# Kernel tuning notes

Hardware: AMD Instinct MI355X
Metric: run time of the kernel (lower is better)

## Reference

```python
import jax, jax.numpy as jnp
import numpy as np

# Config constants (mirrors VQConfig)
N_CODEBOOKS = 4
NUM_EMBS = 512
EMB_DIM = 32
NUM_LATENTS = 64
DECAY = 0.999
COMMITMENT_COST = 0.25
EPSILON = 1e-05
BATCH = 1024


def setup_inputs() -> dict:
    key = jax.random.key(0)
    k1, k2 = jax.random.split(key)
    x = jax.random.normal(k1, (BATCH, N_CODEBOOKS * EMB_DIM * NUM_LATENTS), dtype=jnp.float32)
    # embedding.uniform_(-1/M*5, 1/M*5)
    lim = 5.0 / NUM_EMBS
    embedding = jax.random.uniform(k2, (N_CODEBOOKS, NUM_EMBS, EMB_DIM), dtype=jnp.float32,
                                   minval=-lim, maxval=lim)
    ema_count = jnp.zeros((N_CODEBOOKS, NUM_EMBS), dtype=jnp.float32)
    ema_weight = embedding  # clone of embedding at init
    return {"x": x, "embedding": embedding, "ema_count": ema_count, "ema_weight": ema_weight}


def reference(x, embedding, ema_count, ema_weight):
    N, M, D = embedding.shape
    B = x.shape[0]
    L = x.shape[1] // (N * D)  # num_discrete_latents (H dim; W = 1)
    T = B * L  # flattened positions per codebook

    # x.view(B, N*D, L, 1).view(B, N, D, H, W).permute(1,0,3,4,2) -> [N,B,L,1,D]
    xr = x.reshape(B, N, D, L, 1).transpose(1, 0, 3, 4, 2)
    x_flat = jax.lax.stop_gradient(xr).reshape(N, T, D)

    e_sq = jnp.sum(embedding ** 2, axis=2)                       # [N, M]
    x_sq = jnp.sum(x_flat ** 2, axis=2, keepdims=True)           # [N, T, 1]
    xe = jnp.einsum('ntd,nmd->ntm', x_flat, embedding)           # [N, T, M]
    distances = e_sq[:, None, :] + x_sq - 2.0 * xe
    indices = jnp.argmin(distances, axis=-1)                     # [N, T] int

    # gather: quantized[n, t] = embedding[n, indices[n, t]]
    quantized = jnp.take_along_axis(embedding, indices[..., None], axis=1)  # [N,T,D]
    quantized_r = quantized.reshape(N, B, L, 1, D)

    # one-hot sums without materializing one-hot: scatter-add via segment_sum
    flat_idx = (indices + jnp.arange(N, dtype=indices.dtype)[:, None] * M).reshape(-1)
    counts = jax.ops.segment_sum(jnp.ones((N * T,), jnp.float32), flat_idx,
                                 num_segments=N * M).reshape(N, M)
    dw = jax.ops.segment_sum(x_flat.reshape(N * T, D), flat_idx,
                             num_segments=N * M).reshape(N, M, D)

    # EMA updates (training branch)
    new_ema_count = DECAY * ema_count + (1.0 - DECAY) * counts
    n_tot = jnp.sum(new_ema_count, axis=-1, keepdims=True)
    new_ema_count = (new_ema_count + EPSILON) / (n_tot + M * EPSILON) * n_tot
    new_ema_weight = DECAY * ema_weight + (1.0 - DECAY) * dw
    new_embedding = new_ema_weight / new_ema_count[..., None]

    # commitment loss + straight-through estimator
    e_latent_loss = jnp.mean((xr - jax.lax.stop_gradient(quantized_r)) ** 2)
    loss = COMMITMENT_COST * e_latent_loss
    quantized_st = jax.lax.stop_gradient(quantized_r) + xr - jax.lax.stop_gradient(xr)

    # perplexity
    avg_probs = counts / T                                       # [N, M]
    perplexity = jnp.exp(-jnp.sum(avg_probs * jnp.log(avg_probs + 1e-10), axis=-1))
    perplexity_sum = jnp.sum(perplexity)

    # [N,B,L,1,D] -> permute(1,0,4,2,3) -> [B,N,D,L,1] -> flatten
    z_q = quantized_st.transpose(1, 0, 4, 2, 3).reshape(B, N * D * L)
    indices_out = indices.reshape(N, B, L, 1).transpose(1, 0, 2, 3)  # [B,N,L,1]

    return (z_q, loss, perplexity_sum, indices_out,
            new_embedding, new_ema_count, new_ema_weight)
```

## Files before the change

kernel.cpp:

```cpp
#include <hip/hip_runtime.h>

#define NCB 4
#define M 512
#define D 32
#define L 64
#define B 1024
#define XS (NCB * D * L)

#define ZQ_OFF   0
#define LOSS_OFF 8388608
#define PERP_OFF 8388609
#define IDX_OFF  8388610
#define NEMB_OFF 8650754
#define NEC_OFF  8716290
#define NWE_OFF  8718338

#define WS_COUNTS 0
#define WS_DW     2048
#define WS_SSE    67584
#define WS_ESQ    67585
#define WS_FLOATS (WS_ESQ + NCB * M)

#define REFINE_EPS 1e-4f

#define NP_SUM32(sq, res) do {                                              \
    float r0=(sq)[0], r1=(sq)[1], r2=(sq)[2], r3=(sq)[3];                   \
    float r4=(sq)[4], r5=(sq)[5], r6=(sq)[6], r7=(sq)[7];                   \
    r0 += (sq)[8];  r1 += (sq)[9];  r2 += (sq)[10]; r3 += (sq)[11];         \
    r4 += (sq)[12]; r5 += (sq)[13]; r6 += (sq)[14]; r7 += (sq)[15];         \
    r0 += (sq)[16]; r1 += (sq)[17]; r2 += (sq)[18]; r3 += (sq)[19];         \
    r4 += (sq)[20]; r5 += (sq)[21]; r6 += (sq)[22]; r7 += (sq)[23];         \
    r0 += (sq)[24]; r1 += (sq)[25]; r2 += (sq)[26]; r3 += (sq)[27];         \
    r4 += (sq)[28]; r5 += (sq)[29]; r6 += (sq)[30]; r7 += (sq)[31];         \
    (res) = ((r0 + r1) + (r2 + r3)) + ((r4 + r5) + (r6 + r7));              \
} while (0)

__global__ __launch_bounds__(256) void vq_esq(
    const float* __restrict__ emb, float* __restrict__ ws)
{
#pragma clang fp contract(off)
    const int r = blockIdx.x * 256 + threadIdx.x;
    const float* ep = emb + (size_t)r * D;
    float sq[D];
#pragma unroll
    for (int d = 0; d < D; ++d) { const float e = ep[d]; sq[d] = e * e; }
    float res;
    NP_SUM32(sq, res);
    ws[WS_ESQ + r] = res;
}

__global__ __launch_bounds__(256, 4) void vq_main(
    const float* __restrict__ x, const float* __restrict__ emb,
    const float* __restrict__ esq,
    float* __restrict__ out, float* __restrict__ ws)
{
#pragma clang fp contract(off)
    const int tid = threadIdx.x;
    const int lane = tid & 63;
    const int bid = blockIdx.x;
    const int n  = bid >> 8;
    const int t  = ((bid & 255) << 8) + tid;
    const float* __restrict__ embn = emb + n * (M * D);
    const float* __restrict__ esqn = esq + n * M;

    const int b = t >> 6, l = t & 63;
    float xr[D];
    {
        const float* xp = x + (size_t)b * XS + n * (D * L) + l;
#pragma unroll
        for (int d = 0; d < D; ++d) xr[d] = xp[d * L];
    }

    float xsq;
    {
        float sq[D];
#pragma unroll
        for (int d = 0; d < D; ++d) sq[d] = xr[d] * xr[d];
        NP_SUM32(sq, xsq);
    }

    float best = 3.4e38f, secnd = 3.4e38f;
    int   bi = 0;

    for (int m = 0; m < M; ++m) {
        const float* __restrict__ ep = embn + m * D;
        float a0 = 0.f, a1 = 0.f, a2 = 0.f, a3 = 0.f;
#pragma unroll
        for (int h = 0; h < D; h += 16) {
            a0 = fmaf(ep[h+ 0], xr[h+ 0], a0); a0 = fmaf(ep[h+ 1], xr[h+ 1], a0);
            a0 = fmaf(ep[h+ 2], xr[h+ 2], a0); a0 = fmaf(ep[h+ 3], xr[h+ 3], a0);
            a1 = fmaf(ep[h+ 4], xr[h+ 4], a1); a1 = fmaf(ep[h+ 5], xr[h+ 5], a1);
            a1 = fmaf(ep[h+ 6], xr[h+ 6], a1); a1 = fmaf(ep[h+ 7], xr[h+ 7], a1);
            a2 = fmaf(ep[h+ 8], xr[h+ 8], a2); a2 = fmaf(ep[h+ 9], xr[h+ 9], a2);
            a2 = fmaf(ep[h+10], xr[h+10], a2); a2 = fmaf(ep[h+11], xr[h+11], a2);
            a3 = fmaf(ep[h+12], xr[h+12], a3); a3 = fmaf(ep[h+13], xr[h+13], a3);
            a3 = fmaf(ep[h+14], xr[h+14], a3); a3 = fmaf(ep[h+15], xr[h+15], a3);
        }
        const float s = fmaf(-2.f, ((a0 + a1) + (a2 + a3)), esqn[m]);
        const bool lt = s < best;
        secnd = lt ? best : fminf(secnd, s);
        best  = lt ? s : best;
        bi    = lt ? m : bi;
    }

    {
        unsigned long long mask = __ballot(secnd - best < REFINE_EPS);
        while (mask) {
            const int src = __ffsll(mask) - 1;
            mask &= mask - 1;
            float xb[D];
#pragma unroll
            for (int d = 0; d < D; ++d) xb[d] = __shfl(xr[d], src, 64);
            const float xsb = __shfl(xsq, src, 64);
            float bs = 3.4e38f; int bm = M;
            for (int mb = 0; mb < 8; ++mb) {
                const int m = mb * 64 + lane;
                const float4* e4 = (const float4*)(embn + m * D);
                float ee[D];
#pragma unroll
                for (int q = 0; q < 8; ++q) {
                    const float4 v = e4[q];
                    ee[q*4+0] = v.x; ee[q*4+1] = v.y; ee[q*4+2] = v.z; ee[q*4+3] = v.w;
                }
                float lnk[4];
#pragma unroll
                for (int il = 0; il < 4; ++il) {
                    float c;
                    c = xb[12+il] * ee[12+il];
                    c = xb[ 8+il] * ee[ 8+il] + c;
                    c = xb[ 4+il] * ee[ 4+il] + c;
                    c = xb[ 0+il] * ee[ 0+il] + c;
                    c = xb[28+il] * ee[28+il] + c;
                    c = xb[24+il] * ee[24+il] + c;
                    c = xb[20+il] * ee[20+il] + c;
                    c = xb[16+il] * ee[16+il] + c;
                    lnk[il] = c;
                }
                const float xe   = (lnk[0] + lnk[1]) + (lnk[2] + lnk[3]);
                const float a1v  = esqn[m] + xsb;
                const float dist = a1v - 2.f * xe;
                if (dist < bs || (dist == bs && m < bm)) { bs = dist; bm = m; }
            }
#pragma unroll
            for (int off = 32; off > 0; off >>= 1) {
                const float os = __shfl_xor(bs, off, 64);
                const int   om = __shfl_xor(bm, off, 64);
                if (os < bs || (os == bs && om < bm)) { bs = os; bm = om; }
            }
            if (lane == src) bi = bm;
        }
    }

    float sse = 0.f;
    {
        const float* q = embn + bi * D;
        float* zq = out + ZQ_OFF + (size_t)b * XS + n * (D * L) + l;
#pragma unroll
        for (int d = 0; d < D; ++d) {
            const float qv = q[d];
            zq[d * L] = qv;
            const float diff = xr[d] - qv;
            sse = fmaf(diff, diff, sse);
        }
        out[IDX_OFF + ((size_t)b * NCB + n) * L + l] = (float)bi;
        unsafeAtomicAdd(&ws[WS_COUNTS + n * M + bi], 1.0f);
        float* dwp = ws + WS_DW + (size_t)(n * M + bi) * D;
#pragma unroll
        for (int d = 0; d < D; ++d) unsafeAtomicAdd(&dwp[d], xr[d]);
    }

#pragma unroll
    for (int off = 32; off > 0; off >>= 1) sse += __shfl_down(sse, off, 64);
    if (lane == 0) unsafeAtomicAdd(&ws[WS_SSE], sse);
}

__global__ __launch_bounds__(256) void vq_finalize(
    const float* __restrict__ ema_count, const float* __restrict__ ema_weight,
    const float* __restrict__ ws, float* __restrict__ out)
{
    const int n = blockIdx.x, tid = threadIdx.x;
    __shared__ float s_nec[M];
    __shared__ float s_red[16];

    float pre[2], tot = 0.f, ent = 0.f;
#pragma unroll
    for (int k = 0; k < 2; ++k) {
        const int m = tid + k * 256;
        const float c = ws[WS_COUNTS + n * M + m];
        pre[k] = 0.999f * ema_count[n * M + m] + 0.001f * c;
        tot += pre[k];
        const float p = c * (1.f / 65536.f);
        ent += p * logf(p + 1e-10f);
    }
#pragma unroll
    for (int off = 32; off > 0; off >>= 1) {
        tot += __shfl_down(tot, off, 64);
        ent += __shfl_down(ent, off, 64);
    }
    const int w = tid >> 6;
    if ((tid & 63) == 0) { s_red[w] = tot; s_red[8 + w] = ent; }
    __syncthreads();
    tot = s_red[0] + s_red[1] + s_red[2] + s_red[3];
    ent = s_red[8] + s_red[9] + s_red[10] + s_red[11];

    if (tid == 0) unsafeAtomicAdd(&out[PERP_OFF], expf(-ent));
    if (n == 0 && tid == 0) out[LOSS_OFF] = 0.25f * ws[WS_SSE] * (1.f / 8388608.f);

#pragma unroll
    for (int k = 0; k < 2; ++k) {
        const int m = tid + k * 256;
        const float nec = (pre[k] + 1e-5f) / (tot + M * 1e-5f) * tot;
        out[NEC_OFF + n * M + m] = nec;
        s_nec[m] = nec;
    }
    __syncthreads();

    for (int e = tid; e < M * D; e += 256) {
        const int m = e >> 5;
        const float wv = 0.999f * ema_weight[n * (M * D) + e] + 0.001f * ws[WS_DW + n * (M * D) + e];
        out[NWE_OFF + n * (M * D) + e] = wv;
        out[NEMB_OFF + n * (M * D) + e] = wv / s_nec[m];
    }
}

extern "C" void kernel_launch(void* const* d_in, const int* in_sizes, int n_in,
                              void* d_out, int out_size, void* d_ws, size_t ws_size,
                              hipStream_t stream) {
    const float* x          = (const float*)d_in[0];
    const float* embedding  = (const float*)d_in[1];
    const float* ema_count  = (const float*)d_in[2];
    const float* ema_weight = (const float*)d_in[3];
    float* out = (float*)d_out;
    float* ws  = (float*)d_ws;

    hipMemsetAsync(ws, 0, (WS_SSE + 1) * sizeof(float), stream);
    hipMemsetAsync((char*)d_out + (size_t)LOSS_OFF * sizeof(float), 0, 2 * sizeof(float), stream);

    vq_esq<<<dim3(NCB * M / 256), dim3(256), 0, stream>>>(embedding, ws);
    vq_main<<<dim3(1024), dim3(256), 0, stream>>>(x, embedding, ws + WS_ESQ, out, ws);
    vq_finalize<<<dim3(NCB), dim3(256), 0, stream>>>(ema_count, ema_weight, ws, out);
}
```

Measured before the change: 900.9 us.

## Replace global atomics for counts and dw with LDS-privatized stats kernel

Removes the per-position global atomic adds for code counts and dw sums from the main kernel. A new stats kernel re-reads the indices and x, accumulates dw in shared memory with swizzled atomics across 32 blocks (8 segments per codebook), and writes partial sums that finalize reduces. Counts are now rebuilt in finalize with shared-memory integer atomics. This cuts global atomic contention at the cost of an extra pass over x, an extra launch, and low parallelism (32 blocks for stats, 4 for finalize).

```diff
diff --git a/kernel.cpp b/kernel.cpp
--- a/kernel.cpp
+++ b/kernel.cpp
@@ -15,11 +15,11 @@
 #define NEC_OFF  8716290
 #define NWE_OFF  8718338
 
-#define WS_COUNTS 0
-#define WS_DW     2048
-#define WS_SSE    67584
-#define WS_ESQ    67585
-#define WS_FLOATS (WS_ESQ + NCB * M)
+#define WS_SSE   0
+#define WS_ESQ   1
+#define WS_DWP   (1 + NCB * M)
+#define SBLK     8
+#define SPOS     (65536 / SBLK)
 
 #define REFINE_EPS 1e-4f
 
@@ -163,15 +163,45 @@
             sse = fmaf(diff, diff, sse);
         }
         out[IDX_OFF + ((size_t)b * NCB + n) * L + l] = (float)bi;
-        unsafeAtomicAdd(&ws[WS_COUNTS + n * M + bi], 1.0f);
-        float* dwp = ws + WS_DW + (size_t)(n * M + bi) * D;
-#pragma unroll
-        for (int d = 0; d < D; ++d) unsafeAtomicAdd(&dwp[d], xr[d]);
-    }
-
+    }
 #pragma unroll
     for (int off = 32; off > 0; off >>= 1) sse += __shfl_down(sse, off, 64);
     if (lane == 0) unsafeAtomicAdd(&ws[WS_SSE], sse);
+}
+
+__global__ __launch_bounds__(256) void vq_stats(
+    const float* __restrict__ x, const float* __restrict__ out,
+    float* __restrict__ ws)
+{
+    __shared__ float dwl[M * D];
+    const int tid = threadIdx.x;
+    const int blk = blockIdx.x;
+    const int n = blk >> 3, seg = blk & 7;
+
+#pragma unroll
+    for (int k = 0; k < (M * D) / 256; ++k) dwl[tid + k * 256] = 0.f;
+    __syncthreads();
+
+    const int t0 = seg * SPOS;
+    for (int k = 0; k < SPOS / 256; ++k) {
+        const int t = t0 + k * 256 + tid;
+        const int b = t >> 6, l = t & 63;
+        const int m = (int)out[IDX_OFF + ((size_t)b * NCB + n) * L + l];
+        const float* xp = x + (size_t)b * XS + n * (D * L) + l;
+        const int base = m * D, sw = m & 31;
+#pragma unroll
+        for (int d = 0; d < D; ++d)
+            atomicAdd(&dwl[base + (d ^ sw)], xp[d * L]);
+    }
+    __syncthreads();
+
+    float* dst = ws + WS_DWP + (size_t)(n * SBLK + seg) * (M * D);
+#pragma unroll
+    for (int k = 0; k < (M * D) / 256; ++k) {
+        const int e = tid + k * 256;
+        const int m = e >> 5, d = e & 31;
+        dst[e] = dwl[(e & ~31) + (d ^ (m & 31))];
+    }
 }
 
 __global__ __launch_bounds__(256) void vq_finalize(
@@ -179,14 +209,27 @@
     const float* __restrict__ ws, float* __restrict__ out)
 {
     const int n = blockIdx.x, tid = threadIdx.x;
+    __shared__ int   s_cnt[M];
     __shared__ float s_nec[M];
     __shared__ float s_red[16];
 
+#pragma unroll
+    for (int k = 0; k < 2; ++k) s_cnt[tid + k * 256] = 0;
+    __syncthreads();
+
+    for (int k = 0; k < 65536 / 256; ++k) {
+        const int t = k * 256 + tid;
+        const int b = t >> 6, l = t & 63;
+        const int m = (int)out[IDX_OFF + ((size_t)b * NCB + n) * L + l];
+        atomicAdd(&s_cnt[m], 1);
+    }
+    __syncthreads();
+
     float pre[2], tot = 0.f, ent = 0.f;
 #pragma unroll
     for (int k = 0; k < 2; ++k) {
         const int m = tid + k * 256;
-        const float c = ws[WS_COUNTS + n * M + m];
+        const float c = (float)s_cnt[m];
         pre[k] = 0.999f * ema_count[n * M + m] + 0.001f * c;
         tot += pre[k];
         const float p = c * (1.f / 65536.f);
@@ -216,8 +259,12 @@
     __syncthreads();
 
     for (int e = tid; e < M * D; e += 256) {
+        float dwsum = 0.f;
+#pragma unroll
+        for (int p = 0; p < SBLK; ++p)
+            dwsum += ws[WS_DWP + (size_t)(n * SBLK + p) * (M * D) + e];
         const int m = e >> 5;
-        const float wv = 0.999f * ema_weight[n * (M * D) + e] + 0.001f * ws[WS_DW + n * (M * D) + e];
+        const float wv = 0.999f * ema_weight[n * (M * D) + e] + 0.001f * dwsum;
         out[NWE_OFF + n * (M * D) + e] = wv;
         out[NEMB_OFF + n * (M * D) + e] = wv / s_nec[m];
     }
@@ -233,10 +280,11 @@
     float* out = (float*)d_out;
     float* ws  = (float*)d_ws;
 
-    hipMemsetAsync(ws, 0, (WS_SSE + 1) * sizeof(float), stream);
+    hipMemsetAsync(ws + WS_SSE, 0, sizeof(float), stream);
     hipMemsetAsync((char*)d_out + (size_t)LOSS_OFF * sizeof(float), 0, 2 * sizeof(float), stream);
 
     vq_esq<<<dim3(NCB * M / 256), dim3(256), 0, stream>>>(embedding, ws);
     vq_main<<<dim3(1024), dim3(256), 0, stream>>>(x, embedding, ws + WS_ESQ, out, ws);
+    vq_stats<<<dim3(NCB * SBLK), dim3(256), 0, stream>>>(x, out, ws);
     vq_finalize<<<dim3(NCB), dim3(256), 0, stream>>>(ema_count, ema_weight, ws, out);
 }
```

After: 748.9 us. 1.2x faster.
